# Kernel tuning notes

Measured on AMD Instinct MI355X. Metric: run time of the kernel, lower is better.

Reference implementation:

```python
import jax, jax.numpy as jnp
import numpy as np

# Fixed ViT-B geometry and pool config (match init_kwargs)
P_CLS, L_CLS, K_CLS = 20, 5, 5
P_IMG, L_IMG, K_IMG = 20, 5, 5
P_LEN_CLS = P_CLS * L_CLS          # 100
P_LEN_IMG = P_IMG * L_IMG          # 100
P_LEN = P_LEN_CLS + P_LEN_IMG      # 200
N_TOK = 197                        # 1 cls + 196 patches
N_HEADS = 12
S = N_TOK + P_LEN                  # 397
DIM = 768


def _l2norm(v):
    n = jnp.sqrt(jnp.sum(v * v, axis=-1, keepdims=True))
    return v / jnp.maximum(n, 1e-12)


def _pool(tokens, keys, k):
    # tokens: [N, D], keys: [P, D]
    sim = _l2norm(tokens) @ _l2norm(keys).T            # [N, P]
    vals, idx = jax.lax.top_k(sim, k)                  # gather(sim, topk_idx) == vals
    dist = (1.0 - vals).mean()
    return dist, idx


def setup_inputs() -> dict:
    key = jax.random.key(0)
    k1, k2, k3 = jax.random.split(key, 3)
    x = jax.random.normal(k1, (128, N_TOK, DIM), dtype=jnp.float32)
    keys_cls = jax.random.normal(k2, (12, P_CLS, DIM), dtype=jnp.float32)
    keys_image = jax.random.normal(k3, (12, P_IMG, DIM), dtype=jnp.float32)
    return {"x": x, "keys_cls": keys_cls, "keys_image": keys_image, "layer": 3}


def reference(x, keys_cls, keys_image, layer):
    B = x.shape[0]
    # Base mask rows: cls row sees cls-prompts only; image rows see image-prompts only.
    row_cls = jnp.ones((S,), jnp.float32).at[1 + P_LEN_CLS:1 + P_LEN].set(0.0)
    row_img = jnp.ones((S,), jnp.float32).at[1:1 + P_LEN_CLS].set(0.0)
    base = jnp.concatenate([row_cls[None, :], jnp.tile(row_img, (N_TOK - 1, 1))], axis=0)  # [197, S]
    mask = jnp.broadcast_to(base, (B, N_HEADS, N_TOK, S))

    # CLS token routing -> one-hot over cls pool, expanded per prompt token
    dist_cls, idx_cls = _pool(x[:, 0, :], keys_cls[layer], K_CLS)
    oh_cls = jnp.zeros((B, P_CLS), jnp.float32).at[jnp.arange(B)[:, None], idx_cls].set(1.0)
    tmp_cls = jnp.repeat(oh_cls, L_CLS, axis=1)        # [B, P_LEN_CLS]
    mask = mask.at[:, :, 0, 1:1 + P_LEN_CLS].set(tmp_cls[:, None, :])

    # Image token routing -> per-token one-hot over image pool
    img = x[:, 1:, :].reshape(-1, DIM)                 # [B*196, D]
    dist_img, idx_img = _pool(img, keys_image[layer], K_IMG)
    oh_img = jnp.zeros((B * (N_TOK - 1), P_IMG), jnp.float32)
    oh_img = oh_img.at[jnp.arange(B * (N_TOK - 1))[:, None], idx_img].set(1.0)
    tmp_img = jnp.repeat(oh_img.reshape(B, N_TOK - 1, P_IMG), L_IMG, axis=2)  # [B,196,P_LEN_IMG]
    mask = mask.at[:, :, 1:, 1 + P_LEN_CLS:1 + P_LEN].set(tmp_img[:, None, :, :])

    return mask, dist_cls + dist_img
```

## Files before the change

kernel.cpp:

```cpp
#include <hip/hip_runtime.h>

#define NTOK 197
#define NHEADS 12
#define DIM 768
#define PP 20
#define KK 5
#define STOT 397
#define BB 128
#define NIMG 196
#define NALLTOK (BB * NTOK)
#define HSTRIDE (NTOK * STOT)

static const long long MASK_ELEMS = (long long)BB * NHEADS * NTOK * STOT;

typedef float float4a __attribute__((ext_vector_type(4), aligned(4)));
typedef float float4b __attribute__((ext_vector_type(4), aligned(16)));

static __device__ __forceinline__ float dot4(float4b a, float4b b) {
    return a.x * b.x + a.y * b.y + a.z * b.z + a.w * b.w;
}

__global__ void knorm_kernel(const float* __restrict__ kc,
                             const float* __restrict__ ki,
                             const int* __restrict__ layer_p,
                             float* __restrict__ invn ) {
    int layer = *layer_p;
    int kid = blockIdx.x;
    const float* base = (kid < PP ? kc : ki) + (size_t)layer * PP * DIM;
    const float* kp = base + (size_t)(kid % PP) * DIM;
    int lane = threadIdx.x;
    float s = 0.f;
    for (int i = lane; i < DIM; i += 64) { float v = kp[i]; s += v * v; }
    #pragma unroll
    for (int m = 1; m < 64; m <<= 1) s += __shfl_xor(s, m, 64);
    if (lane == 0) invn[kid] = 1.0f / fmaxf(sqrtf(s), 1e-12f);
}

__global__ __launch_bounds__(64) void fused_kernel(
        const float* __restrict__ x,
        const float* __restrict__ kc,
        const float* __restrict__ ki,
        const int* __restrict__ layer_p,
        const float* __restrict__ invn,
        float* __restrict__ out,
        float* __restrict__ dist_ws ) {
    const int bid = blockIdx.x;
    const int l = threadIdx.x;
    const int b = bid / NTOK;
    const int t = bid - b * NTOK;
    const bool is_cls = (t == 0);
    const int layer = *layer_p;

    const float* __restrict__ kb = (is_cls ? kc : ki) + (size_t)layer * PP * DIM;
    const float* __restrict__ xr = x + (size_t)bid * DIM;

    __shared__ float red[21 * 65 + 64];

    float4b xv0 = *(const float4b*)(xr + 4 * l);
    float4b xv1 = *(const float4b*)(xr + 256 + 4 * l);
    float4b xv2 = *(const float4b*)(xr + 512 + 4 * l);
    float xsq = dot4(xv0, xv0) + dot4(xv1, xv1) + dot4(xv2, xv2);

    float acc[PP];
    #pragma unroll
    for (int p = 0; p < PP; ++p) {
        const float* kp = kb + p * DIM;
        float4b k0 = *(const float4b*)(kp + 4 * l);
        float4b k1 = *(const float4b*)(kp + 256 + 4 * l);
        float4b k2 = *(const float4b*)(kp + 512 + 4 * l);
        acc[p] = dot4(xv0, k0) + dot4(xv1, k1) + dot4(xv2, k2);
    }

    #pragma unroll
    for (int v = 0; v < PP; ++v) red[v * 65 + l] = acc[v];
    red[PP * 65 + l] = xsq;
    __syncthreads();

    float part = 0.f;
    if (l < 63) {
        int r = l / 3;
        int seg = l - 3 * r;
        int s0 = seg * 21 + (seg > 0 ? 1 : 0);
        int n  = 22 - (seg > 0 ? 1 : 0);
        const float* rr = &red[r * 65 + s0];
        #pragma unroll
        for (int i = 0; i < 22; ++i)
            if (i < n) part += rr[i];
    }
    __syncthreads();
    float* red2 = &red[21 * 65];
    if (l < 63) red2[l] = part;
    __syncthreads();

    float dotv = 0.f;
    if (l < 21) dotv = red2[3 * l] + red2[3 * l + 1] + red2[3 * l + 2];

    const float* __restrict__ ik = invn + (is_cls ? 0 : PP);
    float sv = dotv * ((l < PP) ? ik[l] : 1.0f);

    int ibits = __float_as_int(sv);
    unsigned mu = (ibits < 0) ? ~(unsigned)ibits : ((unsigned)ibits | 0x80000000u);

    unsigned su[PP];
    #pragma unroll
    for (int p = 0; p < PP; ++p) su[p] = (unsigned)__builtin_amdgcn_readlane((int)mu, p);
    float xsqv = __uint_as_float((unsigned)__builtin_amdgcn_readlane(__float_as_int(dotv), PP));

    unsigned bits = 0u;
    float sum5 = 0.f;
    #pragma unroll
    for (int j = 0; j < KK; ++j) {
        unsigned best = 0u; int bidx = 0;
        #pragma unroll
        for (int p = 0; p < PP; ++p) {
            bool ok = !((bits >> p) & 1u) && (su[p] > best);
            best = ok ? su[p] : best;
            bidx = ok ? p : bidx;
        }
        bits |= (1u << bidx);
        unsigned fb = (best & 0x80000000u) ? (best & 0x7FFFFFFFu) : ~best;
        sum5 += __uint_as_float(fb);
    }
    float invx = 1.0f / fmaxf(sqrtf(xsqv), 1e-12f);
    if (l == 0) dist_ws[bid] = (float)KK - sum5 * invx;

    const int lo = is_cls ? 1 : 101;
    float4a v0;
    #pragma unroll
    for (int k = 0; k < 4; ++k) {
        int s = 4 * l + k;
        unsigned d = (unsigned)(s - lo);
        bool inw = d < 100u;
        unsigned q = d / 5u;
        float vv = ((s == 0) | (s >= 201)) ? 1.f
                 : (inw ? (float)((bits >> q) & 1u) : 0.f);
        v0[k] = vv;
    }
    float4a ones = {1.f, 1.f, 1.f, 1.f};

    #pragma unroll
    for (int h = 0; h < NHEADS; ++h) {
        float* d0 = out + ((size_t)(b * NHEADS + h) * NTOK + t) * (size_t)STOT;
        *(float4a*)(d0 + 4 * l) = v0;
        if (l < 35)      *(float4a*)(d0 + 256 + 4 * l) = ones;
        else if (l == 35) d0[396] = 1.0f;
    }
}

__global__ __launch_bounds__(256) void reduce_kernel(
        const float* __restrict__ dist_ws,
        float* __restrict__ out) {
    const int tid = threadIdx.x;
    float sc = 0.f, si = 0.f;
    for (int i = tid; i < NALLTOK; i += 256) {
        unsigned q = (unsigned)i / 197u;
        unsigned r = (unsigned)i - q * 197u;
        float v = dist_ws[i];
        if (r == 0) sc += v; else si += v;
    }
    #pragma unroll
    for (int m = 1; m < 64; m <<= 1) {
        sc += __shfl_xor(sc, m, 64);
        si += __shfl_xor(si, m, 64);
    }
    __shared__ float lc[4], li[4];
    int lane = tid & 63, wv = tid >> 6;
    if (lane == 0) { lc[wv] = sc; li[wv] = si; }
    __syncthreads();
    if (tid == 0) {
        float c = lc[0] + lc[1] + lc[2] + lc[3];
        float i = li[0] + li[1] + li[2] + li[3];
        out[MASK_ELEMS] = c / (float)(BB * KK) + i / (float)(BB * NIMG * KK);
    }
}

extern "C" void kernel_launch(void* const* d_in, const int* in_sizes, int n_in,
                              void* d_out, int out_size, void* d_ws, size_t ws_size,
                              hipStream_t stream) {
    const float* x  = (const float*)d_in[0];
    const float* kc = (const float*)d_in[1];
    const float* ki = (const float*)d_in[2];
    const int* layer = (const int*)d_in[3];
    float* out = (float*)d_out;

    float* invn    = (float*)d_ws;
    float* dist_ws = (float*)d_ws + 64;

    knorm_kernel<<<40, 64, 0, stream>>>(kc, ki, layer, invn);
    fused_kernel<<<NALLTOK, 64, 0, stream>>>(x, kc, ki, layer, invn, out, dist_ws);
    reduce_kernel<<<1, 256, 0, stream>>>(dist_ws, out);
}
```

Measured before the change: 229.8 us.

## Split prompt dot products across four waves and use shuffle reductions and nontemporal stores

The fused per-token kernel grows from one wave to four. Each wave computes dot products against five of the twenty keys and reduces them with cross-lane shuffles instead of the two-stage shared-memory transpose reduction. The mask rows are now written with scalar nontemporal stores, one element per thread, replacing the unaligned float4 stores. This aims to cut per-block latency and improve write behaviour on a store-bound kernel, at the cost of more threads per block and narrower stores.

```diff
diff --git a/kernel.cpp b/kernel.cpp
--- a/kernel.cpp
+++ b/kernel.cpp
@@ -13,7 +13,6 @@
 
 static const long long MASK_ELEMS = (long long)BB * NHEADS * NTOK * STOT;
 
-typedef float float4a __attribute__((ext_vector_type(4), aligned(4)));
 typedef float float4b __attribute__((ext_vector_type(4), aligned(16)));
 
 static __device__ __forceinline__ float dot4(float4b a, float4b b) {
@@ -36,7 +35,7 @@
     if (lane == 0) invn[kid] = 1.0f / fmaxf(sqrtf(s), 1e-12f);
 }
 
-__global__ __launch_bounds__(64) void fused_kernel(
+__global__ __launch_bounds__(256) void fused_kernel(
         const float* __restrict__ x,
         const float* __restrict__ kc,
         const float* __restrict__ ki,
@@ -45,7 +44,9 @@
         float* __restrict__ out,
         float* __restrict__ dist_ws ) {
     const int bid = blockIdx.x;
-    const int l = threadIdx.x;
+    const int tid = threadIdx.x;
+    const int l = tid & 63;
+    const int w = tid >> 6;
     const int b = bid / NTOK;
     const int t = bid - b * NTOK;
     const bool is_cls = (t == 0);
@@ -54,52 +55,43 @@
     const float* __restrict__ kb = (is_cls ? kc : ki) + (size_t)layer * PP * DIM;
     const float* __restrict__ xr = x + (size_t)bid * DIM;
 
-    __shared__ float red[21 * 65 + 64];
+    __shared__ float vals[24];
 
     float4b xv0 = *(const float4b*)(xr + 4 * l);
     float4b xv1 = *(const float4b*)(xr + 256 + 4 * l);
     float4b xv2 = *(const float4b*)(xr + 512 + 4 * l);
-    float xsq = dot4(xv0, xv0) + dot4(xv1, xv1) + dot4(xv2, xv2);
 
-    float acc[PP];
+    float acc[5];
     #pragma unroll
-    for (int p = 0; p < PP; ++p) {
-        const float* kp = kb + p * DIM;
+    for (int j = 0; j < 5; ++j) {
+        const float* kp = kb + (size_t)(5 * w + j) * DIM;
         float4b k0 = *(const float4b*)(kp + 4 * l);
         float4b k1 = *(const float4b*)(kp + 256 + 4 * l);
         float4b k2 = *(const float4b*)(kp + 512 + 4 * l);
-        acc[p] = dot4(xv0, k0) + dot4(xv1, k1) + dot4(xv2, k2);
+        acc[j] = dot4(xv0, k0) + dot4(xv1, k1) + dot4(xv2, k2);
     }
-
     #pragma unroll
-    for (int v = 0; v < PP; ++v) red[v * 65 + l] = acc[v];
-    red[PP * 65 + l] = xsq;
+    for (int m = 1; m < 64; m <<= 1) {
+        #pragma unroll
+        for (int j = 0; j < 5; ++j) acc[j] += __shfl_xor(acc[j], m, 64);
+    }
+    if (w == 0) {
+        float xsq = dot4(xv0, xv0) + dot4(xv1, xv1) + dot4(xv2, xv2);
+        #pragma unroll
+        for (int m = 1; m < 64; m <<= 1) xsq += __shfl_xor(xsq, m, 64);
+        if (l == 0) vals[PP] = xsq;
+    }
+    if (l == 0) {
+        #pragma unroll
+        for (int j = 0; j < 5; ++j) vals[5 * w + j] = acc[j];
+    }
     __syncthreads();
 
-    float part = 0.f;
-    if (l < 63) {
-        int r = l / 3;
-        int seg = l - 3 * r;
-        int s0 = seg * 21 + (seg > 0 ? 1 : 0);
-        int n  = 22 - (seg > 0 ? 1 : 0);
-        const float* rr = &red[r * 65 + s0];
-        #pragma unroll
-        for (int i = 0; i < 22; ++i)
-            if (i < n) part += rr[i];
-    }
-    __syncthreads();
-    float* red2 = &red[21 * 65];
-    if (l < 63) red2[l] = part;
-    __syncthreads();
-
-    float dotv = 0.f;
-    if (l < 21) dotv = red2[3 * l] + red2[3 * l + 1] + red2[3 * l + 2];
-
-    const float* __restrict__ ik = invn + (is_cls ? 0 : PP);
-    float sv = dotv * ((l < PP) ? ik[l] : 1.0f);
-
-    int ibits = __float_as_int(sv);
-    unsigned mu = (ibits < 0) ? ~(unsigned)ibits : ((unsigned)ibits | 0x80000000u);
+    float dotv = vals[l < 21 ? l : 20];
+    float ikl = (l < PP) ? invn[(is_cls ? 0 : PP) + l] : 1.0f;
+    float sv = dotv * ikl;
+    int ib = __float_as_int(sv);
+    unsigned mu = (ib < 0) ? ~(unsigned)ib : ((unsigned)ib | 0x80000000u);
 
     unsigned su[PP];
     #pragma unroll
@@ -122,28 +114,21 @@
         sum5 += __uint_as_float(fb);
     }
     float invx = 1.0f / fmaxf(sqrtf(xsqv), 1e-12f);
-    if (l == 0) dist_ws[bid] = (float)KK - sum5 * invx;
+    if (tid == 0) dist_ws[bid] = (float)KK - sum5 * invx;
 
     const int lo = is_cls ? 1 : 101;
-    float4a v0;
-    #pragma unroll
-    for (int k = 0; k < 4; ++k) {
-        int s = 4 * l + k;
-        unsigned d = (unsigned)(s - lo);
-        bool inw = d < 100u;
-        unsigned q = d / 5u;
-        float vv = ((s == 0) | (s >= 201)) ? 1.f
-                 : (inw ? (float)((bits >> q) & 1u) : 0.f);
-        v0[k] = vv;
-    }
-    float4a ones = {1.f, 1.f, 1.f, 1.f};
-
+    unsigned d = (unsigned)(tid - lo);
+    bool inw = d < 100u;
+    unsigned q = d / 5u;
+    float v1 = ((tid == 0) | (tid >= 201)) ? 1.f
+             : (inw ? (float)((bits >> q) & 1u) : 0.f);
+    const bool act2 = tid < (STOT - 256);
+    float* base = out + ((size_t)(b * NHEADS) * NTOK + t) * (size_t)STOT;
     #pragma unroll
     for (int h = 0; h < NHEADS; ++h) {
-        float* d0 = out + ((size_t)(b * NHEADS + h) * NTOK + t) * (size_t)STOT;
-        *(float4a*)(d0 + 4 * l) = v0;
-        if (l < 35)      *(float4a*)(d0 + 256 + 4 * l) = ones;
-        else if (l == 35) d0[396] = 1.0f;
+        float* d0 = base + (size_t)h * HSTRIDE;
+        __builtin_nontemporal_store(v1, d0 + tid);
+        if (act2) __builtin_nontemporal_store(1.0f, d0 + tid + 256);
     }
 }
 
@@ -153,8 +138,8 @@
     const int tid = threadIdx.x;
     float sc = 0.f, si = 0.f;
     for (int i = tid; i < NALLTOK; i += 256) {
-        unsigned q = (unsigned)i / 197u;
-        unsigned r = (unsigned)i - q * 197u;
+        unsigned qq = (unsigned)i / 197u;
+        unsigned r = (unsigned)i - qq * 197u;
         float v = dist_ws[i];
         if (r == 0) sc += v; else si += v;
     }
@@ -187,6 +172,6 @@
     float* dist_ws = (float*)d_ws + 64;
 
     knorm_kernel<<<40, 64, 0, stream>>>(kc, ki, layer, invn);
-    fused_kernel<<<NALLTOK, 64, 0, stream>>>(x, kc, ki, layer, invn, out, dist_ws);
+    fused_kernel<<<NALLTOK, 256, 0, stream>>>(x, kc, ki, layer, invn, out, dist_ws);
     reduce_kernel<<<1, 256, 0, stream>>>(dist_ws, out);
 }
```

Result: faster. 209.6 us (-8.8%).
